# Optimization experiments

Measured on AMD Instinct MI355X. Metric: run time of the kernel, lower is better.

The kernel has to match this reference:

```python
import jax, jax.numpy as jnp
import numpy as np

NUM_HEADS = 16
HEAD_DIM = 128
MODEL_DIM = 2048
SEQ = 4096
INIT = 0.02


def setup_inputs() -> dict:
    key = jax.random.key(0)
    k1, k2, k3 = jax.random.split(key, 3)
    x = jax.random.normal(k1, (SEQ, MODEL_DIM), dtype=jnp.float32)
    w_attn = jax.random.normal(k2, (MODEL_DIM, 3 * MODEL_DIM), dtype=jnp.float32) * INIT
    b_attn = jnp.zeros((3 * MODEL_DIM,), dtype=jnp.float32)
    w_proj = jax.random.normal(k3, (MODEL_DIM, MODEL_DIM), dtype=jnp.float32) * INIT
    b_proj = jnp.zeros((MODEL_DIM,), dtype=jnp.float32)
    return {"x": x, "w_attn": w_attn, "b_attn": b_attn, "w_proj": w_proj, "b_proj": b_proj}


def reference(x, w_attn, b_attn, w_proj, b_proj):
    seq = x.shape[0]
    # fused QKV projection: [seq, 3*model_dim]
    hidden = x @ w_attn + b_attn
    q, k, v = jnp.split(hidden, 3, axis=-1)
    q = q.reshape(seq, NUM_HEADS, HEAD_DIM)
    k = k.reshape(seq, NUM_HEADS, HEAD_DIM)
    v = v.reshape(seq, NUM_HEADS, HEAD_DIM)
    q = q / jnp.sqrt(jnp.asarray(HEAD_DIM, dtype=q.dtype))
    # scores: [heads, q, k]
    scores = jnp.einsum('qhd,khd->hqk', q, k)
    causal = jnp.tril(jnp.ones((seq, seq), dtype=bool))  # mask[q, k]
    big_neg = jnp.finfo(jnp.float32).min
    scores = jnp.where(causal[None, :, :], scores, big_neg)
    pattern = jax.nn.softmax(scores, axis=-1)
    z = jnp.einsum('hqk,khd->qhd', pattern, v)
    out = z.reshape(seq, MODEL_DIM) @ w_proj + b_proj
    return out
```

## Files before the change

### kernel.cpp

```cpp
#include <hip/hip_runtime.h>
#include <hip/hip_bf16.h>
#include <stdint.h>
#include <stddef.h>

typedef __bf16 bf16_8 __attribute__((ext_vector_type(8)));
typedef __bf16 bf16_4 __attribute__((ext_vector_type(4)));
typedef float f32x4 __attribute__((ext_vector_type(4)));

#define BIG_NEG (-1e30f)
#define QSCALE (0.08838834764831845f * 1.4426950408889634f)
#define FIXMAX 16.0f

__device__ __forceinline__ void gld_lds16(const void* g, void* l) {
  __builtin_amdgcn_global_load_lds(
      (const __attribute__((address_space(1))) uint32_t*)g,
      (__attribute__((address_space(3))) uint32_t*)l, 16, 0, 0);
}

#define BAR()                      \
  do {                             \
    asm volatile("" ::: "memory"); \
    __builtin_amdgcn_s_barrier();  \
    asm volatile("" ::: "memory"); \
  } while (0)

__global__ __launch_bounds__(256) void convert_bf16(
    const float* __restrict__ in, __bf16* __restrict__ out, long long n) {
  long long i = ((long long)blockIdx.x * 256 + threadIdx.x) * 8;
  if (i + 8 > n) return;
  const float4* in4 = (const float4*)(in + i);
  float4 a = in4[0], b = in4[1];
  bf16_8 o = {(__bf16)a.x, (__bf16)a.y, (__bf16)a.z, (__bf16)a.w,
              (__bf16)b.x, (__bf16)b.y, (__bf16)b.z, (__bf16)b.w};
  *(bf16_8*)(out + i) = o;
}

__global__ __launch_bounds__(256) void transpose_cvt(
    const float* __restrict__ in, __bf16* __restrict__ out, int R, int C) {
  __shared__ __bf16 tile[32][33];
  int bx = blockIdx.x * 32;
  int by = blockIdx.y * 32;
  int tx = threadIdx.x;
  int ty = threadIdx.y;
#pragma unroll
  for (int j = 0; j < 32; j += 8)
    tile[ty + j][tx] = (__bf16)in[(size_t)(by + ty + j) * C + bx + tx];
  __syncthreads();
#pragma unroll
  for (int j = 0; j < 32; j += 8)
    out[(size_t)(bx + ty + j) * R + by + tx] = tile[tx][ty + j];
}

__global__ __launch_bounds__(512, 2) void gemm_bt256(
    const __bf16* __restrict__ A, const __bf16* __restrict__ Bt,
    const float* __restrict__ bias, __bf16* __restrict__ C0,
    __bf16* __restrict__ VT, float* __restrict__ Cf,
    int M, int N, int K, int mode) {
  __shared__ __bf16 As[2][128 * 64];
  __shared__ __bf16 Bs[2][256 * 64];

  const int t = threadIdx.x;
  const int lane = t & 63;
  const int wave = t >> 6;
  const int col = lane & 15;
  const int quad = lane >> 4;
  const int wr = wave >> 2;
  const int wc = wave & 3;
  const int m0 = blockIdx.y * 128;
  const int n0 = blockIdx.x * 256;
  const bool vswap = (mode == 1) && (n0 >= 4096);

  const int trow = t >> 3;
  const int sk = (((trow & 7) ^ (t & 7)) * 8);
  const __bf16* gA = A + (size_t)(m0 + trow) * K + sk;
  const __bf16* gB = Bt + (size_t)(n0 + trow) * K + sk;
  const int ldst = wave * 512;

  const int ar = wr * 64 + col;
  const int br = wc * 64 + col;
  const int sq0 = ((quad) ^ (col & 7)) * 8;
  const int sq1 = ((quad ^ 4) ^ (col & 7)) * 8;

  f32x4 acc[4][4];
#pragma unroll
  for (int i = 0; i < 4; i++)
#pragma unroll
    for (int j = 0; j < 4; j++) acc[i][j] = f32x4{0.f, 0.f, 0.f, 0.f};

  const int nk = K / 64;

#define STA(b, L, kk) \
  gld_lds16(gA + (size_t)(L) * 64 * K + (kk), &As[b][(L) * 4096 + ldst])
#define STB(b, L, kk) \
  gld_lds16(gB + (size_t)(L) * 64 * K + (kk), &Bs[b][(L) * 4096 + ldst])

#define RDA(c)                                                         \
  do {                                                                 \
    afp[0] = *(const bf16_8*)(&As[cb][(ar + (c) * 16) * 64 + sq0]);    \
    afp[1] = *(const bf16_8*)(&As[cb][(ar + (c) * 16) * 64 + sq1]);    \
  } while (0)

#define CL(c)                                                          \
  do {                                                                 \
    if (!vswap) {                                                      \
      _Pragma("unroll") for (int ni = 0; ni < 4; ++ni) {               \
        acc[(c)][ni] = __builtin_amdgcn_mfma_f32_16x16x32_bf16(        \
            afp[0], bfr[ni][0], acc[(c)][ni], 0, 0, 0);                \
        acc[(c)][ni] = __builtin_amdgcn_mfma_f32_16x16x32_bf16(        \
            afp[1], bfr[ni][1], acc[(c)][ni], 0, 0, 0);                \
      }                                                                \
    } else {                                                           \
      _Pragma("unroll") for (int ni = 0; ni < 4; ++ni) {               \
        acc[(c)][ni] = __builtin_amdgcn_mfma_f32_16x16x32_bf16(        \
            bfr[ni][0], afp[0], acc[(c)][ni], 0, 0, 0);                \
        acc[(c)][ni] = __builtin_amdgcn_mfma_f32_16x16x32_bf16(        \
            bfr[ni][1], afp[1], acc[(c)][ni], 0, 0, 0);                \
      }                                                                \
    }                                                                  \
  } while (0)

#define LGKM0()                                       \
  do {                                                \
    asm volatile("s_waitcnt lgkmcnt(0)" ::: "memory");\
    __builtin_amdgcn_sched_barrier(0);                \
  } while (0)

  STA(0, 0, 0); STA(0, 1, 0);
  STB(0, 0, 0); STB(0, 1, 0); STB(0, 2, 0); STB(0, 3, 0);
  STA(1, 0, 64); STA(1, 1, 64);
  STB(1, 0, 64); STB(1, 1, 64); STB(1, 2, 64); STB(1, 3, 64);
  asm volatile("s_waitcnt vmcnt(6)" ::: "memory");
  BAR();

  for (int kt = 0; kt < nk; ++kt) {
    const int cb = kt & 1;
    const int kk = (kt + 2) * 64;
    const bool st = (kt + 2) < nk;

    bf16_8 bfr[4][2], afp[2];
#pragma unroll
    for (int ni = 0; ni < 4; ++ni) {
      bfr[ni][0] = *(const bf16_8*)(&Bs[cb][(br + ni * 16) * 64 + sq0]);
      bfr[ni][1] = *(const bf16_8*)(&Bs[cb][(br + ni * 16) * 64 + sq1]);
    }
    RDA(0);
    LGKM0();
    __builtin_amdgcn_s_setprio(1);
    CL(0);
    __builtin_amdgcn_s_setprio(0);

    BAR();
    if (st) { STB(cb, 0, kk); STB(cb, 1, kk); STB(cb, 2, kk); STB(cb, 3, kk); }

    RDA(1);
    LGKM0();
    __builtin_amdgcn_s_setprio(1);
    CL(1);
    __builtin_amdgcn_s_setprio(0);

    RDA(2);
    LGKM0();
    __builtin_amdgcn_s_setprio(1);
    CL(2);
    __builtin_amdgcn_s_setprio(0);

    RDA(3);
    LGKM0();
    BAR();
    if (st) { STA(cb, 0, kk); STA(cb, 1, kk); }
    __builtin_amdgcn_sched_barrier(0);
    __builtin_amdgcn_s_setprio(1);
    CL(3);
    __builtin_amdgcn_s_setprio(0);

    if (st)
      asm volatile("s_waitcnt vmcnt(6)" ::: "memory");
    else
      asm volatile("s_waitcnt vmcnt(0)" ::: "memory");
    BAR();
  }
#undef STA
#undef STB
#undef RDA
#undef CL
#undef LGKM0

  if (mode == 0) {
#pragma unroll
    for (int mi = 0; mi < 4; mi++)
#pragma unroll
      for (int ni = 0; ni < 4; ni++) {
        int gn = n0 + wc * 64 + ni * 16 + col;
        float bv = bias[gn];
#pragma unroll
        for (int r = 0; r < 4; r++)
          Cf[(size_t)(m0 + wr * 64 + mi * 16 + quad * 4 + r) * N + gn] =
              acc[mi][ni][r] + bv;
      }
  } else if (n0 < 2048) {
#pragma unroll
    for (int mi = 0; mi < 4; mi++)
#pragma unroll
      for (int ni = 0; ni < 4; ni++) {
        int gn = n0 + wc * 64 + ni * 16 + col;
        float bv = bias[gn];
#pragma unroll
        for (int r = 0; r < 4; r++)
          C0[(size_t)(m0 + wr * 64 + mi * 16 + quad * 4 + r) * 4096 + gn] =
              (__bf16)((acc[mi][ni][r] + bv) * QSCALE);
      }
  } else if (n0 < 4096) {
#pragma unroll
    for (int mi = 0; mi < 4; mi++)
#pragma unroll
      for (int ni = 0; ni < 4; ni++) {
        int gn = n0 + wc * 64 + ni * 16 + col;
        float bv = bias[gn];
#pragma unroll
        for (int r = 0; r < 4; r++)
          C0[(size_t)(m0 + wr * 64 + mi * 16 + quad * 4 + r) * 4096 + gn] =
              (__bf16)(acc[mi][ni][r] + bv);
      }
  } else {
#pragma unroll
    for (int mi = 0; mi < 4; mi++) {
      int seq = m0 + wr * 64 + mi * 16 + col;
#pragma unroll
      for (int ni = 0; ni < 4; ni++) {
#pragma unroll
        for (int r = 0; r < 4; r++) {
          int gn = n0 + wc * 64 + ni * 16 + quad * 4 + r;
          float bv = bias[gn];
          VT[(size_t)(gn - 4096) * M + seq] = (__bf16)(acc[mi][ni][r] + bv);
        }
      }
    }
  }
}

__global__ __launch_bounds__(256, 2) void flash_attn(
    const __bf16* __restrict__ QK, const __bf16* __restrict__ VT,
    __bf16* __restrict__ Z, uint32_t* __restrict__ cnt) {
  constexpr int KS = 136;
  constexpr int VS = 72;
  constexpr int PS = 72;
  __shared__ __bf16 Ks[64 * KS];
  __shared__ __bf16 Vs[128 * VS];
  __shared__ __bf16 Ps[4 * 2 * 16 * PS];
  __shared__ int s_task;

  const int t = threadIdx.x;
  const int lane = t & 63;
  const int wave = t >> 6;
  const int col = lane & 15;
  const int quad = lane >> 4;

  __bf16* kdst = Ks + (t >> 4) * KS + (t & 15) * 8;
  __bf16* vdst = Vs + (t >> 3) * VS + (t & 7) * 8;
  __bf16* pw0 = Ps + (wave * 2 + 0) * 16 * PS;
  __bf16* pw1 = Ps + (wave * 2 + 1) * 16 * PS;

  for (;;) {
    if (t == 0) s_task = (int)atomicAdd(cnt, 1u);
    __syncthreads();
    const int tau = s_task;
    if (tau >= 512) return;
    const int ta = 31 - (tau >> 4);
    const int h = tau & 15;
    const int q0 = ta * 128;
    const int nkb = 2 * (ta + 1);

    const __bf16* kbase =
        QK + (size_t)(t >> 4) * 4096 + 2048 + h * 128 + (t & 15) * 8;
    const __bf16* vbase =
        VT + (size_t)(h * 128 + (t >> 3)) * 4096 + (t & 7) * 8;

    bf16_8 qf[4][2];
#pragma unroll
    for (int qg = 0; qg < 2; qg++) {
      const __bf16* qp =
          QK + (size_t)(q0 + wave * 32 + qg * 16 + col) * 4096 + h * 128;
#pragma unroll
      for (int i = 0; i < 4; i++)
        qf[i][qg] = *(const bf16_8*)(qp + i * 32 + quad * 8);
    }

    f32x4 z[8][2];
#pragma unroll
    for (int i = 0; i < 8; i++) {
      z[i][0] = f32x4{0.f, 0.f, 0.f, 0.f};
      z[i][1] = f32x4{0.f, 0.f, 0.f, 0.f};
    }
    float lsum[2] = {0.f, 0.f};

    bf16_8 kpre[4], vpre[4];
#pragma unroll
    for (int j = 0; j < 4; j++) {
      kpre[j] = *(const bf16_8*)(kbase + (size_t)j * 16 * 4096);
      vpre[j] = *(const bf16_8*)(vbase + (size_t)j * 32 * 4096);
    }

    for (int kb = 0; kb < nkb; kb++) {
      const int k0 = kb * 64;
      __syncthreads();
#pragma unroll
      for (int j = 0; j < 4; j++) {
        *(bf16_8*)(kdst + j * 16 * KS) = kpre[j];
        *(bf16_8*)(vdst + j * 32 * VS) = vpre[j];
      }
      __syncthreads();

      if (kb + 1 < nkb) {
        const __bf16* kb2 = kbase + (size_t)(k0 + 64) * 4096;
        const __bf16* vb2 = vbase + (k0 + 64);
#pragma unroll
        for (int j = 0; j < 4; j++) {
          kpre[j] = *(const bf16_8*)(kb2 + (size_t)j * 16 * 4096);
          vpre[j] = *(const bf16_8*)(vb2 + (size_t)j * 32 * 4096);
        }
      }

      f32x4 sh[4][2];
      __builtin_amdgcn_s_setprio(1);
#pragma unroll
      for (int p = 0; p < 4; p++) {
        sh[p][0] = f32x4{0.f, 0.f, 0.f, 0.f};
        sh[p][1] = f32x4{0.f, 0.f, 0.f, 0.f};
#pragma unroll
        for (int kd = 0; kd < 4; kd++) {
          bf16_8 kf =
              *(const bf16_8*)(Ks + (p * 16 + col) * KS + kd * 32 + quad * 8);
          sh[p][0] = __builtin_amdgcn_mfma_f32_16x16x32_bf16(kf, qf[kd][0],
                                                             sh[p][0], 0, 0, 0);
          sh[p][1] = __builtin_amdgcn_mfma_f32_16x16x32_bf16(kf, qf[kd][1],
                                                             sh[p][1], 0, 0, 0);
        }
      }
      __builtin_amdgcn_s_setprio(0);

      if (kb >= nkb - 2) {
#pragma unroll
        for (int qg = 0; qg < 2; qg++) {
          int qgl = q0 + wave * 32 + qg * 16 + col;
#pragma unroll
          for (int p = 0; p < 4; p++)
#pragma unroll
            for (int r = 0; r < 4; r++)
              if (k0 + p * 16 + quad * 4 + r > qgl) sh[p][qg][r] = BIG_NEG;
        }
      }

#pragma unroll
      for (int qg = 0; qg < 2; qg++) {
        __bf16* pw = qg ? pw1 : pw0;
        float rs = 0.f;
#pragma unroll
        for (int p = 0; p < 4; p++) {
          float e0 = exp2f(sh[p][qg][0] - FIXMAX);
          float e1 = exp2f(sh[p][qg][1] - FIXMAX);
          float e2 = exp2f(sh[p][qg][2] - FIXMAX);
          float e3 = exp2f(sh[p][qg][3] - FIXMAX);
          rs += (e0 + e1) + (e2 + e3);
          bf16_4 pk = {(__bf16)e0, (__bf16)e1, (__bf16)e2, (__bf16)e3};
          *(bf16_4*)(pw + col * PS + p * 16 + quad * 4) = pk;
        }
        lsum[qg] += rs;
      }

      bf16_8 pf0a = *(const bf16_8*)(pw0 + col * PS + quad * 8);
      bf16_8 pf0b = *(const bf16_8*)(pw0 + col * PS + 32 + quad * 8);
      bf16_8 pf1a = *(const bf16_8*)(pw1 + col * PS + quad * 8);
      bf16_8 pf1b = *(const bf16_8*)(pw1 + col * PS + 32 + quad * 8);

      __builtin_amdgcn_s_setprio(1);
#pragma unroll
      for (int db = 0; db < 8; db++) {
        bf16_8 vf0 = *(const bf16_8*)(Vs + (db * 16 + col) * VS + quad * 8);
        z[db][0] = __builtin_amdgcn_mfma_f32_16x16x32_bf16(vf0, pf0a, z[db][0],
                                                           0, 0, 0);
        z[db][1] = __builtin_amdgcn_mfma_f32_16x16x32_bf16(vf0, pf1a, z[db][1],
                                                           0, 0, 0);
        bf16_8 vf1 =
            *(const bf16_8*)(Vs + (db * 16 + col) * VS + 32 + quad * 8);
        z[db][0] = __builtin_amdgcn_mfma_f32_16x16x32_bf16(vf1, pf0b, z[db][0],
                                                           0, 0, 0);
        z[db][1] = __builtin_amdgcn_mfma_f32_16x16x32_bf16(vf1, pf1b, z[db][1],
                                                           0, 0, 0);
      }
      __builtin_amdgcn_s_setprio(0);
    }

#pragma unroll
    for (int qg = 0; qg < 2; qg++) {
      float l = lsum[qg];
      l += __shfl_xor(l, 16, 64);
      l += __shfl_xor(l, 32, 64);
      float rl = 1.f / l;
      __bf16* zrow = Z + (size_t)(q0 + wave * 32 + qg * 16 + col) * 2048 +
                     h * 128 + quad * 4;
#pragma unroll
      for (int db = 0; db < 8; db++) {
        bf16_4 o = {(__bf16)(z[db][qg][0] * rl), (__bf16)(z[db][qg][1] * rl),
                    (__bf16)(z[db][qg][2] * rl), (__bf16)(z[db][qg][3] * rl)};
        *(bf16_4*)(zrow + db * 16) = o;
      }
    }
  }
}

extern "C" void kernel_launch(void* const* d_in, const int* in_sizes, int n_in,
                              void* d_out, int out_size, void* d_ws,
                              size_t ws_size, hipStream_t stream) {
  const float* x = (const float*)d_in[0];
  const float* w_attn = (const float*)d_in[1];
  const float* b_attn = (const float*)d_in[2];
  const float* w_proj = (const float*)d_in[3];
  const float* b_proj = (const float*)d_in[4];
  float* out = (float*)d_out;

  __bf16* ws = (__bf16*)d_ws;
  __bf16* QK = ws;
  __bf16* VT = ws + 16777216;
  __bf16* WT1 = ws + 25165824;
  __bf16* Zb = ws + 25165824;
  uint32_t* cnt = (uint32_t*)(ws + 33554432);
  __bf16* WT2 = ws + 37748736;
  __bf16* xb = ws + 41943040;

  convert_bf16<<<4096, 256, 0, stream>>>(x, xb, 8388608LL);
  transpose_cvt<<<dim3(6144 / 32, 2048 / 32), dim3(32, 8), 0, stream>>>(
      w_attn, WT1, 2048, 6144);
  transpose_cvt<<<dim3(2048 / 32, 2048 / 32), dim3(32, 8), 0, stream>>>(
      w_proj, WT2, 2048, 2048);

  gemm_bt256<<<dim3(6144 / 256, 4096 / 128), 512, 0, stream>>>(
      xb, WT1, b_attn, QK, VT, nullptr, 4096, 6144, 2048, 1);

  hipMemsetAsync((void*)cnt, 0, 4, stream);
  flash_attn<<<dim3(384), 256, 0, stream>>>(QK, VT, Zb, cnt);

  gemm_bt256<<<dim3(2048 / 256, 4096 / 128), 512, 0, stream>>>(
      Zb, WT2, b_proj, nullptr, nullptr, out, 4096, 2048, 2048, 0);
}
```

Baseline: 465.3 us.

## Split long causal attention tiles across KV range with atomic fp32 combine

Query tiles in the upper half of the sequence (ta >= 16) are split into two tasks over halves of their key range. Each half atomically accumulates unnormalized fp32 partial outputs and row sums into a zeroed buffer, and a new combine_z kernel normalizes the result and writes bf16 Z. Shorter tiles stay whole and write normalized bf16 output directly. The grid grows to 512 blocks and the task table orders work longest-first, with the aim of better load balance and more parallelism. In exchange it adds a 16 MB memset, many global float atomics, an extra kernel launch, and nondeterministic summation order; this depends on the fixed softmax max offset making partial sums additive.

```diff
diff --git a/kernel.cpp b/kernel.cpp
--- a/kernel.cpp
+++ b/kernel.cpp
@@ -240,7 +240,8 @@
 
 __global__ __launch_bounds__(256, 2) void flash_attn(
     const __bf16* __restrict__ QK, const __bf16* __restrict__ VT,
-    __bf16* __restrict__ Z, uint32_t* __restrict__ cnt) {
+    __bf16* __restrict__ Z, uint32_t* __restrict__ cnt,
+    float* __restrict__ zf32, float* __restrict__ lbuf) {
   constexpr int KS = 136;
   constexpr int VS = 72;
   constexpr int PS = 72;
@@ -249,6 +250,12 @@
   __shared__ __bf16 Ps[4 * 2 * 16 * PS];
   __shared__ int s_task;
 
+  static const uint8_t TT[48] = {
+      31, 95, 143, 30, 94, 29, 93, 142, 28, 92, 27, 91, 141, 26, 90, 25,
+      89, 140, 24, 88, 23, 87, 139, 22, 86, 21, 85, 138, 20, 84, 19, 83,
+      137, 18, 82, 17, 81, 136, 16, 80, 135, 134, 133, 132, 131, 130, 129,
+      128};
+
   const int t = threadIdx.x;
   const int lane = t & 63;
   const int wave = t >> 6;
@@ -264,11 +271,14 @@
     if (t == 0) s_task = (int)atomicAdd(cnt, 1u);
     __syncthreads();
     const int tau = s_task;
-    if (tau >= 512) return;
-    const int ta = 31 - (tau >> 4);
+    if (tau >= 768) return;
+    const uint32_t v = TT[tau >> 4];
     const int h = tau & 15;
+    const int ta = v & 63;
+    const bool fullT = (v & 128) != 0;
+    const int kb0 = (v & 64) ? (ta + 1) : 0;
+    const int kb1 = (fullT || (v & 64)) ? (2 * ta + 2) : (ta + 1);
     const int q0 = ta * 128;
-    const int nkb = 2 * (ta + 1);
 
     const __bf16* kbase =
         QK + (size_t)(t >> 4) * 4096 + 2048 + h * 128 + (t & 15) * 8;
@@ -296,11 +306,11 @@
     bf16_8 kpre[4], vpre[4];
 #pragma unroll
     for (int j = 0; j < 4; j++) {
-      kpre[j] = *(const bf16_8*)(kbase + (size_t)j * 16 * 4096);
-      vpre[j] = *(const bf16_8*)(vbase + (size_t)j * 32 * 4096);
-    }
-
-    for (int kb = 0; kb < nkb; kb++) {
+      kpre[j] = *(const bf16_8*)(kbase + ((size_t)kb0 * 64 + j * 16) * 4096);
+      vpre[j] = *(const bf16_8*)(vbase + (size_t)j * 32 * 4096 + kb0 * 64);
+    }
+
+    for (int kb = kb0; kb < kb1; kb++) {
       const int k0 = kb * 64;
       __syncthreads();
 #pragma unroll
@@ -310,7 +320,7 @@
       }
       __syncthreads();
 
-      if (kb + 1 < nkb) {
+      if (kb + 1 < kb1) {
         const __bf16* kb2 = kbase + (size_t)(k0 + 64) * 4096;
         const __bf16* vb2 = vbase + (k0 + 64);
 #pragma unroll
@@ -338,7 +348,7 @@
       }
       __builtin_amdgcn_s_setprio(0);
 
-      if (kb >= nkb - 2) {
+      if (kb >= 2 * ta) {
 #pragma unroll
         for (int qg = 0; qg < 2; qg++) {
           int qgl = q0 + wave * 32 + qg * 16 + col;
@@ -390,22 +400,52 @@
       __builtin_amdgcn_s_setprio(0);
     }
 
-#pragma unroll
-    for (int qg = 0; qg < 2; qg++) {
-      float l = lsum[qg];
-      l += __shfl_xor(l, 16, 64);
-      l += __shfl_xor(l, 32, 64);
-      float rl = 1.f / l;
-      __bf16* zrow = Z + (size_t)(q0 + wave * 32 + qg * 16 + col) * 2048 +
-                     h * 128 + quad * 4;
-#pragma unroll
-      for (int db = 0; db < 8; db++) {
-        bf16_4 o = {(__bf16)(z[db][qg][0] * rl), (__bf16)(z[db][qg][1] * rl),
-                    (__bf16)(z[db][qg][2] * rl), (__bf16)(z[db][qg][3] * rl)};
-        *(bf16_4*)(zrow + db * 16) = o;
+    if (!fullT) {
+#pragma unroll
+      for (int qg = 0; qg < 2; qg++) {
+        float l = lsum[qg];
+        l += __shfl_xor(l, 16, 64);
+        l += __shfl_xor(l, 32, 64);
+        int qrow = q0 + wave * 32 + qg * 16 + col;
+        if (quad == 0) atomicAdd(&lbuf[(size_t)(qrow - 2048) * 16 + h], l);
+        float* zr = zf32 + (size_t)(qrow - 2048) * 2048 + h * 128 + quad * 4;
+#pragma unroll
+        for (int db = 0; db < 8; db++)
+#pragma unroll
+          for (int r = 0; r < 4; r++)
+            atomicAdd(zr + db * 16 + r, z[db][qg][r]);
+      }
+    } else {
+#pragma unroll
+      for (int qg = 0; qg < 2; qg++) {
+        float l = lsum[qg];
+        l += __shfl_xor(l, 16, 64);
+        l += __shfl_xor(l, 32, 64);
+        float rl = 1.f / l;
+        __bf16* zrow = Z + (size_t)(q0 + wave * 32 + qg * 16 + col) * 2048 +
+                       h * 128 + quad * 4;
+#pragma unroll
+        for (int db = 0; db < 8; db++) {
+          bf16_4 o = {(__bf16)(z[db][qg][0] * rl), (__bf16)(z[db][qg][1] * rl),
+                      (__bf16)(z[db][qg][2] * rl), (__bf16)(z[db][qg][3] * rl)};
+          *(bf16_4*)(zrow + db * 16) = o;
+        }
       }
     }
   }
+}
+
+__global__ __launch_bounds__(256) void combine_z(
+    const float* __restrict__ zf, const float* __restrict__ lb,
+    __bf16* __restrict__ Z) {
+  int i = (blockIdx.x * 256 + threadIdx.x) * 4;
+  int row = i >> 11;
+  int colb = i & 2047;
+  float rl = 1.f / lb[(row << 4) + (colb >> 7)];
+  float4 v = *(const float4*)(zf + i);
+  bf16_4 o = {(__bf16)(v.x * rl), (__bf16)(v.y * rl), (__bf16)(v.z * rl),
+              (__bf16)(v.w * rl)};
+  *(bf16_4*)(Z + (size_t)(2048 + row) * 2048 + colb) = o;
 }
 
 extern "C" void kernel_launch(void* const* d_in, const int* in_sizes, int n_in,
@@ -423,9 +463,11 @@
   __bf16* VT = ws + 16777216;
   __bf16* WT1 = ws + 25165824;
   __bf16* Zb = ws + 25165824;
-  uint32_t* cnt = (uint32_t*)(ws + 33554432);
+  float* lbuf = (float*)(ws + 33554432);
+  uint32_t* cnt = (uint32_t*)(ws + 33554432 + 65536);
   __bf16* WT2 = ws + 37748736;
   __bf16* xb = ws + 41943040;
+  float* zf32 = (float*)(ws + 41943040);
 
   convert_bf16<<<4096, 256, 0, stream>>>(x, xb, 8388608LL);
   transpose_cvt<<<dim3(6144 / 32, 2048 / 32), dim3(32, 8), 0, stream>>>(
@@ -436,8 +478,11 @@
   gemm_bt256<<<dim3(6144 / 256, 4096 / 128), 512, 0, stream>>>(
       xb, WT1, b_attn, QK, VT, nullptr, 4096, 6144, 2048, 1);
 
-  hipMemsetAsync((void*)cnt, 0, 4, stream);
-  flash_attn<<<dim3(384), 256, 0, stream>>>(QK, VT, Zb, cnt);
+  hipMemsetAsync((void*)zf32, 0, 2048 * 2048 * 4, stream);
+  hipMemsetAsync((void*)lbuf, 0, 2048 * 16 * 4 + 4, stream);
+
+  flash_attn<<<dim3(512), 256, 0, stream>>>(QK, VT, Zb, cnt, zf32, lbuf);
+  combine_z<<<dim3(4096), 256, 0, stream>>>(zf32, lbuf, Zb);
 
   gemm_bt256<<<dim3(2048 / 256, 4096 / 128), 512, 0, stream>>>(
       Zb, WT2, b_proj, nullptr, nullptr, out, 4096, 2048, 2048, 0);
```

Result: slower. 530.9 us (+14.1%).
